# Kernel tuning notes

Hardware: AMD Instinct MI355X
Metric: run time of the kernel (lower is better)

## Reference

```python
import jax, jax.numpy as jnp
import numpy as np

HEADS = 12


def setup_inputs() -> dict:
    key = jax.random.key(0)
    ks = jax.random.split(key, 3)
    B, N, C = 4, 2048, 768
    x = jax.random.normal(ks[0], (B, N, C), dtype=jnp.float32)
    Wqkv = jax.random.normal(ks[1], (C, 3 * C), dtype=jnp.float32) * 0.02
    bqkv = jnp.zeros((3 * C,), dtype=jnp.float32)
    Wproj = jax.random.normal(ks[2], (C, C), dtype=jnp.float32) * 0.02
    bproj = jnp.zeros((C,), dtype=jnp.float32)
    return {"x": x, "Wqkv": Wqkv, "bqkv": bqkv, "Wproj": Wproj, "bproj": bproj}


def reference(x, Wqkv, bqkv, Wproj, bproj):
    B, N, C = x.shape
    h = HEADS
    d = C // h
    scale = d ** (-0.5)
    # QKV projection: (B, N, 3C) -> (3, B, h, N, d)
    qkv = (x @ Wqkv + bqkv).reshape(B, N, 3, h, d).transpose(2, 0, 3, 1, 4)
    q, k, v = qkv[0], qkv[1], qkv[2]
    # Full N x N attention scores per head (matches original explicit matmul)
    scores = jnp.einsum("bhnd,bhmd->bhnm", q, k) * scale
    attn = jax.nn.softmax(scores, axis=-1)
    out = jnp.einsum("bhnm,bhmd->bhnd", attn, v)  # (B, h, N, d)
    out = out.transpose(0, 2, 1, 3).reshape(B, N, C)
    return out @ Wproj + bproj
```

## Files before the change

### kernel.cpp

```cpp
#include <hip/hip_runtime.h>
#include <hip/hip_bf16.h>
#include <math.h>

#define B_ 4
#define N_ 2048
#define C_ 768
#define H_ 12
#define D_ 64
#define SC_LOG2E 0.18033688f

typedef __attribute__((ext_vector_type(8))) short bf16x8;
typedef __attribute__((ext_vector_type(4))) short bf16x4;
typedef __attribute__((ext_vector_type(4))) float f32x4;

#define MFMA16(A, B, C)  __builtin_amdgcn_mfma_f32_16x16x32_bf16(A, B, C, 0, 0, 0)
#define MFMAK16(A, B, C) __builtin_amdgcn_mfma_f32_16x16x16bf16_1k(A, B, C, 0, 0, 0)

#if __has_builtin(__builtin_amdgcn_exp2f)
#define EXP2F(x) __builtin_amdgcn_exp2f(x)
#else
#define EXP2F(x) exp2f(x)
#endif

__device__ __forceinline__ ushort f2bf(float f) {
    union { float f; unsigned u; } v; v.f = f;
    unsigned r = v.u + 0x7fffu + ((v.u >> 16) & 1u);
    return (ushort)(r >> 16);
}

#if __has_builtin(__builtin_amdgcn_cvt_pk_bf16_f32)
typedef __attribute__((ext_vector_type(2))) __bf16 bf16x2v;
__device__ __forceinline__ unsigned pack_bf2(float a, float b) {
    union { bf16x2v v; unsigned u; } cv;
    cv.v = __builtin_amdgcn_cvt_pk_bf16_f32(a, b);
    return cv.u;
}
#else
__device__ __forceinline__ unsigned pack_bf2(float a, float b) {
    union { __hip_bfloat162 h2; unsigned u; } cv;
    cv.h2 = __float22bfloat162_rn(make_float2(a, b));
    return cv.u;
}
#endif

__device__ __forceinline__ void gl_lds16(const ushort* g, ushort* l) {
    __builtin_amdgcn_global_load_lds(
        (const __attribute__((address_space(1))) unsigned*)g,
        (__attribute__((address_space(3))) unsigned*)l, 16, 0, 0);
}

__global__ __launch_bounds__(256) void cvt_x(const float* __restrict__ x,
                                             ushort* __restrict__ xb) {
    int i = blockIdx.x * 256 + threadIdx.x;
    const float4* p = (const float4*)x + 2 * (size_t)i;
    float4 a = p[0], bq = p[1];
    union { ushort s[8]; uint4 v; } u;
    u.s[0] = f2bf(a.x);  u.s[1] = f2bf(a.y);  u.s[2] = f2bf(a.z);  u.s[3] = f2bf(a.w);
    u.s[4] = f2bf(bq.x); u.s[5] = f2bf(bq.y); u.s[6] = f2bf(bq.z); u.s[7] = f2bf(bq.w);
    *(uint4*)&xb[(size_t)i * 8] = u.v;
}

__global__ __launch_bounds__(256) void tr_cvt(const float* __restrict__ W,
                                              ushort* __restrict__ Wt, int K, int N) {
    __shared__ float T[32][33];
    int t = threadIdx.x;
    int k0 = blockIdx.y * 32, n0 = blockIdx.x * 32;
    int r = t >> 3, c4 = (t & 7) * 4;
    float4 v = *(const float4*)&W[(size_t)(k0 + r) * N + n0 + c4];
    T[r][c4] = v.x; T[r][c4 + 1] = v.y; T[r][c4 + 2] = v.z; T[r][c4 + 3] = v.w;
    __syncthreads();
    union { ushort s[4]; unsigned long long u; } o;
    o.s[0] = f2bf(T[c4 + 0][r]);
    o.s[1] = f2bf(T[c4 + 1][r]);
    o.s[2] = f2bf(T[c4 + 2][r]);
    o.s[3] = f2bf(T[c4 + 3][r]);
    *(unsigned long long*)&Wt[(size_t)(n0 + r) * K + k0 + c4] = o.u;
}

__global__ __launch_bounds__(256) void vtrans(const ushort* __restrict__ qkvb,
                                              ushort* __restrict__ Vt) {
    __shared__ ushort T[64 * 64];
    const int tid = threadIdx.x;
    const int t0 = blockIdx.x * 64, bh = blockIdx.y;
    const int b = bh / H_, h = bh % H_;
#pragma unroll
    for (int i = 0; i < 2; i++) {
        int c = i * 256 + tid;
        int tok = c >> 3, dc = c & 7;
        uint4 v = *(const uint4*)&qkvb[((size_t)b * N_ + t0 + tok) * (3 * C_)
                                       + 2 * C_ + h * D_ + dc * 8];
        const ushort* vs = (const ushort*)&v;
#pragma unroll
        for (int j = 0; j < 8; j++) {
            int d = dc * 8 + j;
            int sc = (tok >> 3) ^ (d & 7) ^ (d >> 3);
            T[d * 64 + sc * 8 + (tok & 7)] = vs[j];
        }
    }
    __syncthreads();
#pragma unroll
    for (int i = 0; i < 2; i++) {
        int c = i * 256 + tid;
        int d = c >> 3, tc = c & 7;
        int sc = tc ^ (d & 7) ^ (d >> 3);
        uint4 o = *(const uint4*)&T[d * 64 + sc * 8];
        *(uint4*)&Vt[((size_t)bh * D_ + d) * N_ + t0 + tc * 8] = o;
    }
}

template <bool OBF>
__global__ __launch_bounds__(256) void gemm_bf16(
    const ushort* __restrict__ A, const ushort* __restrict__ Bt,
    const float* __restrict__ bias, void* __restrict__ outp,
    int M, int N, int K)
{
    __shared__ ushort Asl[128 * 32];
    __shared__ ushort Bsl[128 * 32];

    const int tid  = threadIdx.x;
    const int lane = tid & 63, w = tid >> 6;
    const int quad = lane >> 4, l16 = lane & 15;
    const int row0 = blockIdx.y * 128, col0 = blockIdx.x * 128;
    const int mh = (w >> 1) * 64, nh = (w & 1) * 64;
    const int sw = (quad ^ (l16 & 3)) * 8;

    f32x4 acc[4][4];
#pragma unroll
    for (int i = 0; i < 4; i++)
#pragma unroll
        for (int j = 0; j < 4; j++) acc[i][j] = (f32x4)0.f;

    for (int k0 = 0; k0 < K; k0 += 32) {
#pragma unroll
        for (int i = 0; i < 2; i++) {
            int c  = i * 256 + w * 64 + lane;
            int rr = c >> 2;
            int cc = (c & 3) ^ (rr & 3);
            int wb = (i * 256 + w * 64) * 8;
            gl_lds16(&A[(size_t)(row0 + rr) * K + k0 + cc * 8], &Asl[wb]);
            gl_lds16(&Bt[(size_t)(col0 + rr) * K + k0 + cc * 8], &Bsl[wb]);
        }
        __syncthreads();
        bf16x8 af[4], bfr[4];
#pragma unroll
        for (int mt = 0; mt < 4; mt++)
            af[mt] = *(const bf16x8*)&Asl[(mh + mt * 16 + l16) * 32 + sw];
#pragma unroll
        for (int nt = 0; nt < 4; nt++)
            bfr[nt] = *(const bf16x8*)&Bsl[(nh + nt * 16 + l16) * 32 + sw];
#pragma unroll
        for (int mt = 0; mt < 4; mt++)
#pragma unroll
            for (int nt = 0; nt < 4; nt++)
                acc[mt][nt] = MFMA16(af[mt], bfr[nt], acc[mt][nt]);
        __syncthreads();
    }

    const float scl = (OBF && col0 < C_) ? SC_LOG2E : 1.f;
#pragma unroll
    for (int nt = 0; nt < 4; nt++) {
        int col = col0 + nh + nt * 16 + l16;
        float bv = bias[col];
#pragma unroll
        for (int mt = 0; mt < 4; mt++) {
            f32x4 v = acc[mt][nt];
#pragma unroll
            for (int r = 0; r < 4; r++) {
                int row = row0 + mh + mt * 16 + quad * 4 + r;
                if (OBF)
                    ((ushort*)outp)[(size_t)row * N + col] = f2bf((v[r] + bv) * scl);
                else
                    ((float*)outp)[(size_t)row * N + col] = v[r] + bv;
            }
        }
    }
}

__global__ __launch_bounds__(256) void attn_mfma(
    const ushort* __restrict__ qkvb, const ushort* __restrict__ Vt,
    ushort* __restrict__ attnb)
{
    __shared__ ushort Kd[2][64 * 64];
    __shared__ ushort Vd[2][64 * 64];

    const int tid  = threadIdx.x;
    const int lane = tid & 63, w = tid >> 6;
    const int quad = lane >> 4, l16 = lane & 15;
    const int bh = blockIdx.y, b = bh / H_, h = bh % H_;
    const int q0 = blockIdx.x * 128 + w * 32;
    const size_t rowbase = (size_t)b * N_;
    const int hoff = h * D_;
    const f32x4 Z4 = {0.f, 0.f, 0.f, 0.f};

    const ushort* Kg = qkvb + rowbase * (3 * C_) + C_ + hoff;
    const ushort* Vg = Vt + (size_t)bh * D_ * N_;

    int rr0, cc0, rr1, cc1, wb0, wb1;
    {
        int c0 = w * 64 + lane, c1 = 256 + w * 64 + lane;
        rr0 = c0 >> 3; cc0 = (c0 & 7) ^ (rr0 & 7); wb0 = (w * 64) * 8;
        rr1 = c1 >> 3; cc1 = (c1 & 7) ^ (rr1 & 7); wb1 = (256 + w * 64) * 8;
    }
    const ushort* kp0 = Kg + (size_t)rr0 * (3 * C_) + cc0 * 8;
    const ushort* kp1 = Kg + (size_t)rr1 * (3 * C_) + cc1 * 8;
    const ushort* vp0 = Vg + (size_t)rr0 * N_ + cc0 * 8;
    const ushort* vp1 = Vg + (size_t)rr1 * N_ + cc1 * 8;

    bf16x8 Qf[2][2];
#pragma unroll
    for (int qt = 0; qt < 2; qt++)
#pragma unroll
        for (int c = 0; c < 2; c++)
            Qf[qt][c] = *(const bf16x8*)&qkvb[(rowbase + q0 + qt * 16 + l16) * (3 * C_)
                                              + hoff + c * 32 + quad * 8];

    f32x4 oacc[4][2];
#pragma unroll
    for (int dt = 0; dt < 4; dt++)
#pragma unroll
        for (int qt = 0; qt < 2; qt++) oacc[dt][qt] = (f32x4)0.f;
    float lrow[2] = {0.f, 0.f};

    gl_lds16(kp0, &Kd[0][wb0]);
    gl_lds16(vp0, &Vd[0][wb0]);
    gl_lds16(kp1, &Kd[0][wb1]);
    gl_lds16(vp1, &Vd[0][wb1]);
    kp0 += 64 * 3 * C_; kp1 += 64 * 3 * C_; vp0 += 64; vp1 += 64;
    __syncthreads();

#define TILE_BODY(CB, PREFETCH)                                               \
    {                                                                         \
        if (PREFETCH) {                                                       \
            gl_lds16(kp0, &Kd[(CB) ^ 1][wb0]);                                \
            gl_lds16(vp0, &Vd[(CB) ^ 1][wb0]);                                \
            gl_lds16(kp1, &Kd[(CB) ^ 1][wb1]);                                \
            gl_lds16(vp1, &Vd[(CB) ^ 1][wb1]);                                \
        }                                                                     \
        kp0 += 64 * 3 * C_; kp1 += 64 * 3 * C_; vp0 += 64; vp1 += 64;         \
        f32x4 sacc[4][2];                                                     \
        {                              \
            bf16x8 kf[4];                                                     \
            _Pragma("unroll")                                                 \
            for (int kt = 0; kt < 4; kt++)                                    \
                kf[kt] = *(const bf16x8*)&Kd[CB][(kt * 16 + l16) * 64         \
                                               + ((quad) ^ (l16 & 7)) * 8];   \
            _Pragma("unroll")                                                 \
            for (int kt = 0; kt < 4; kt++)                                    \
                _Pragma("unroll")                                             \
                for (int qt = 0; qt < 2; qt++)                                \
                    sacc[kt][qt] = MFMA16(kf[kt], Qf[qt][0], Z4);             \
        }                                                                     \
        {                                            \
            bf16x8 kf[4];                                                     \
            _Pragma("unroll")                                                 \
            for (int kt = 0; kt < 4; kt++)                                    \
                kf[kt] = *(const bf16x8*)&Kd[CB][(kt * 16 + l16) * 64         \
                                               + ((4 | quad) ^ (l16 & 7)) * 8]; \
            _Pragma("unroll")                                                 \
            for (int kt = 0; kt < 4; kt++)                                    \
                _Pragma("unroll")                                             \
                for (int qt = 0; qt < 2; qt++)                                \
                    sacc[kt][qt] = MFMA16(kf[kt], Qf[qt][1], sacc[kt][qt]);   \
        }                                                                     \
        union { unsigned u[2]; bf16x4 v; } pf[2][4];                          \
        _Pragma("unroll")                                                     \
        for (int qt = 0; qt < 2; qt++) {                                      \
            float sum = 0.f;                                                  \
            _Pragma("unroll")                                                 \
            for (int kt = 0; kt < 4; kt++) {                                  \
                float p0 = EXP2F(sacc[kt][qt][0]);                            \
                float p1 = EXP2F(sacc[kt][qt][1]);                            \
                float p2 = EXP2F(sacc[kt][qt][2]);                            \
                float p3 = EXP2F(sacc[kt][qt][3]);                            \
                sum += (p0 + p1) + (p2 + p3);                                 \
                pf[qt][kt].u[0] = pack_bf2(p0, p1);                           \
                pf[qt][kt].u[1] = pack_bf2(p2, p3);                           \
            }                                                                 \
            lrow[qt] += sum;                                                  \
        }                                                                     \
        _Pragma("unroll")                                                     \
        for (int c16 = 0; c16 < 4; c16++) {                                   \
               \
            const int vcol = ((2 * c16 + (quad >> 1)) ^ (l16 & 7)) * 8        \
                             + (quad & 1) * 4;                                \
            _Pragma("unroll")                                                 \
            for (int dt = 0; dt < 4; dt++) {                                  \
                bf16x4 vf = *(const bf16x4*)&Vd[CB][(dt * 16 + l16) * 64 + vcol]; \
                _Pragma("unroll")                                             \
                for (int qt = 0; qt < 2; qt++)                                \
                    oacc[dt][qt] = MFMAK16(vf, pf[qt][c16].v, oacc[dt][qt]);  \
            }                                                                 \
        }                                                                     \
        __syncthreads();                                                      \
    }

    for (int tt = 0; tt < 16; tt++) {
        TILE_BODY(0, 1)
        TILE_BODY(1, (tt < 15))
    }
#undef TILE_BODY

#pragma unroll
    for (int qt = 0; qt < 2; qt++) {
        float s = lrow[qt];
        s += __shfl_xor(s, 16, 64);
        s += __shfl_xor(s, 32, 64);
        float inv = 1.f / s;
        size_t orow = (rowbase + q0 + qt * 16 + l16) * C_ + hoff;
#pragma unroll
        for (int dt = 0; dt < 4; dt++) {
            union { ushort us[4]; unsigned long long u; } o;
#pragma unroll
            for (int r = 0; r < 4; r++) o.us[r] = f2bf(oacc[dt][qt][r] * inv);
            *(unsigned long long*)&attnb[orow + dt * 16 + quad * 4] = o.u;
        }
    }
}

extern "C" void kernel_launch(void* const* d_in, const int* in_sizes, int n_in,
                              void* d_out, int out_size, void* d_ws, size_t ws_size,
                              hipStream_t stream)
{
    const float* x     = (const float*)d_in[0];
    const float* Wqkv  = (const float*)d_in[1];
    const float* bqkv  = (const float*)d_in[2];
    const float* Wproj = (const float*)d_in[3];
    const float* bproj = (const float*)d_in[4];

    ushort* xb     = (ushort*)d_ws;
    ushort* Wqkvt  = xb + (size_t)B_ * N_ * C_;
    ushort* Wprojt = Wqkvt + (size_t)3 * C_ * C_;
    ushort* qkvb   = Wprojt + (size_t)C_ * C_;
    ushort* attnb  = qkvb + (size_t)B_ * N_ * 3 * C_;
    ushort* Vtb    = attnb + (size_t)B_ * N_ * C_;

    const int M = B_ * N_;

    cvt_x<<<(M * C_) / (8 * 256), 256, 0, stream>>>(x, xb);
    tr_cvt<<<dim3((3 * C_) / 32, C_ / 32), 256, 0, stream>>>(Wqkv, Wqkvt, C_, 3 * C_);
    tr_cvt<<<dim3(C_ / 32, C_ / 32), 256, 0, stream>>>(Wproj, Wprojt, C_, C_);

    gemm_bf16<true><<<dim3((3 * C_) / 128, M / 128), 256, 0, stream>>>(
        xb, Wqkvt, bqkv, qkvb, M, 3 * C_, C_);

    vtrans<<<dim3(N_ / 64, B_ * H_), 256, 0, stream>>>(qkvb, Vtb);

    attn_mfma<<<dim3(N_ / 128, B_ * H_), 256, 0, stream>>>(qkvb, Vtb, attnb);

    gemm_bf16<false><<<dim3(C_ / 128, M / 128), 256, 0, stream>>>(
        attnb, Wprojt, bproj, d_out, M, C_, C_);
}
```

Before: 252.6 us.

## Stage P through LDS for K=32 MFMA in PV and merge prep kernels

The three prep kernels (x conversion and two weight transposes) are merged into one launch that dispatches on block index, removing two launch gaps. In attention, P probabilities are written to a per-wave padded LDS tile and read back in 8-element fragments. This lets the PV product use the 16x16x32 bf16 MFMA with 8-wide V loads in place of the 16x16x16 variant with 4-wide loads, halving the MFMA count for that product. The cost is extra LDS traffic and a write-then-read round trip for P within each wave, plus extra LDS footprint.

Result: no change. 248.9 us (-1.5%).

```diff
diff --git a/kernel.cpp b/kernel.cpp
--- a/kernel.cpp
+++ b/kernel.cpp
@@ -10,11 +10,9 @@
 #define SC_LOG2E 0.18033688f
 
 typedef __attribute__((ext_vector_type(8))) short bf16x8;
-typedef __attribute__((ext_vector_type(4))) short bf16x4;
 typedef __attribute__((ext_vector_type(4))) float f32x4;
 
-#define MFMA16(A, B, C)  __builtin_amdgcn_mfma_f32_16x16x32_bf16(A, B, C, 0, 0, 0)
-#define MFMAK16(A, B, C) __builtin_amdgcn_mfma_f32_16x16x16bf16_1k(A, B, C, 0, 0, 0)
+#define MFMA16(A, B, C) __builtin_amdgcn_mfma_f32_16x16x32_bf16(A, B, C, 0, 0, 0)
 
 #if __has_builtin(__builtin_amdgcn_exp2f)
 #define EXP2F(x) __builtin_amdgcn_exp2f(x)
@@ -49,22 +47,11 @@
         (__attribute__((address_space(3))) unsigned*)l, 16, 0, 0);
 }
 
-__global__ __launch_bounds__(256) void cvt_x(const float* __restrict__ x,
-                                             ushort* __restrict__ xb) {
-    int i = blockIdx.x * 256 + threadIdx.x;
-    const float4* p = (const float4*)x + 2 * (size_t)i;
-    float4 a = p[0], bq = p[1];
-    union { ushort s[8]; uint4 v; } u;
-    u.s[0] = f2bf(a.x);  u.s[1] = f2bf(a.y);  u.s[2] = f2bf(a.z);  u.s[3] = f2bf(a.w);
-    u.s[4] = f2bf(bq.x); u.s[5] = f2bf(bq.y); u.s[6] = f2bf(bq.z); u.s[7] = f2bf(bq.w);
-    *(uint4*)&xb[(size_t)i * 8] = u.v;
-}
-
-__global__ __launch_bounds__(256) void tr_cvt(const float* __restrict__ W,
-                                              ushort* __restrict__ Wt, int K, int N) {
+__device__ __forceinline__ void tr_body(const float* __restrict__ W,
+                                        ushort* __restrict__ Wt,
+                                        int K, int N, int bx, int by, int t) {
     __shared__ float T[32][33];
-    int t = threadIdx.x;
-    int k0 = blockIdx.y * 32, n0 = blockIdx.x * 32;
+    int k0 = by * 32, n0 = bx * 32;
     int r = t >> 3, c4 = (t & 7) * 4;
     float4 v = *(const float4*)&W[(size_t)(k0 + r) * N + n0 + c4];
     T[r][c4] = v.x; T[r][c4 + 1] = v.y; T[r][c4 + 2] = v.z; T[r][c4 + 3] = v.w;
@@ -77,6 +64,29 @@
     *(unsigned long long*)&Wt[(size_t)(n0 + r) * K + k0 + c4] = o.u;
 }
 
+__global__ __launch_bounds__(256) void prep(
+    const float* __restrict__ x, ushort* __restrict__ xb,
+    const float* __restrict__ Wqkv, ushort* __restrict__ Wqkvt,
+    const float* __restrict__ Wproj, ushort* __restrict__ Wprojt)
+{
+    const int bid = blockIdx.x, t = threadIdx.x;
+    if (bid < 3072) {
+        int i = bid * 256 + t;
+        const float4* p = (const float4*)x + 2 * (size_t)i;
+        float4 a = p[0], bq = p[1];
+        union { ushort s[8]; uint4 v; } u;
+        u.s[0] = f2bf(a.x);  u.s[1] = f2bf(a.y);  u.s[2] = f2bf(a.z);  u.s[3] = f2bf(a.w);
+        u.s[4] = f2bf(bq.x); u.s[5] = f2bf(bq.y); u.s[6] = f2bf(bq.z); u.s[7] = f2bf(bq.w);
+        *(uint4*)&xb[(size_t)i * 8] = u.v;
+    } else if (bid < 4800) {
+        int id = bid - 3072;
+        tr_body(Wqkv, Wqkvt, C_, 3 * C_, id % 72, id / 72, t);
+    } else {
+        int id = bid - 4800;
+        tr_body(Wproj, Wprojt, C_, C_, id % 24, id / 24, t);
+    }
+}
+
 __global__ __launch_bounds__(256) void vtrans(const ushort* __restrict__ qkvb,
                                               ushort* __restrict__ Vt) {
     __shared__ ushort T[64 * 64];
@@ -182,6 +192,7 @@
 {
     __shared__ ushort Kd[2][64 * 64];
     __shared__ ushort Vd[2][64 * 64];
+    __shared__ ushort Ptl[4 * 32 * 72];
 
     const int tid  = threadIdx.x;
     const int lane = tid & 63, w = tid >> 6;
@@ -190,6 +201,7 @@
     const int q0 = blockIdx.x * 128 + w * 32;
     const size_t rowbase = (size_t)b * N_;
     const int hoff = h * D_;
+    ushort* Ptw = Ptl + w * 32 * 72;
     const f32x4 Z4 = {0.f, 0.f, 0.f, 0.f};
 
     const ushort* Kg = qkvb + rowbase * (3 * C_) + C_ + hoff;
@@ -238,7 +250,7 @@
         }                                                                     \
         kp0 += 64 * 3 * C_; kp1 += 64 * 3 * C_; vp0 += 64; vp1 += 64;         \
         f32x4 sacc[4][2];                                                     \
-        {                              \
+        {                                \
             bf16x8 kf[4];                                                     \
             _Pragma("unroll")                                                 \
             for (int kt = 0; kt < 4; kt++)                                    \
@@ -250,7 +262,7 @@
                 for (int qt = 0; qt < 2; qt++)                                \
                     sacc[kt][qt] = MFMA16(kf[kt], Qf[qt][0], Z4);             \
         }                                                                     \
-        {                                            \
+        {                                              \
             bf16x8 kf[4];                                                     \
             _Pragma("unroll")                                                 \
             for (int kt = 0; kt < 4; kt++)                                    \
@@ -262,7 +274,6 @@
                 for (int qt = 0; qt < 2; qt++)                                \
                     sacc[kt][qt] = MFMA16(kf[kt], Qf[qt][1], sacc[kt][qt]);   \
         }                                                                     \
-        union { unsigned u[2]; bf16x4 v; } pf[2][4];                          \
         _Pragma("unroll")                                                     \
         for (int qt = 0; qt < 2; qt++) {                                      \
             float sum = 0.f;                                                  \
@@ -273,22 +284,27 @@
                 float p2 = EXP2F(sacc[kt][qt][2]);                            \
                 float p3 = EXP2F(sacc[kt][qt][3]);                            \
                 sum += (p0 + p1) + (p2 + p3);                                 \
-                pf[qt][kt].u[0] = pack_bf2(p0, p1);                           \
-                pf[qt][kt].u[1] = pack_bf2(p2, p3);                           \
+                uint2 pk;                                                     \
+                pk.x = pack_bf2(p0, p1);                                      \
+                pk.y = pack_bf2(p2, p3);                                      \
+                *(uint2*)&Ptw[(qt * 16 + l16) * 72 + kt * 16 + quad * 4] = pk; \
             }                                                                 \
             lrow[qt] += sum;                                                  \
         }                                                                     \
         _Pragma("unroll")                                                     \
-        for (int c16 = 0; c16 < 4; c16++) {                                   \
-               \
-            const int vcol = ((2 * c16 + (quad >> 1)) ^ (l16 & 7)) * 8        \
-                             + (quad & 1) * 4;                                \
+        for (int c = 0; c < 2; c++) {                                         \
+            bf16x8 pf[2];                                                     \
+            _Pragma("unroll")                                                 \
+            for (int qt = 0; qt < 2; qt++)                                    \
+                pf[qt] = *(const bf16x8*)&Ptw[(qt * 16 + l16) * 72            \
+                                              + c * 32 + quad * 8];           \
             _Pragma("unroll")                                                 \
             for (int dt = 0; dt < 4; dt++) {                                  \
-                bf16x4 vf = *(const bf16x4*)&Vd[CB][(dt * 16 + l16) * 64 + vcol]; \
+                bf16x8 vf = *(const bf16x8*)&Vd[CB][(dt * 16 + l16) * 64      \
+                                   + (((c << 2) | quad) ^ (l16 & 7)) * 8];    \
                 _Pragma("unroll")                                             \
                 for (int qt = 0; qt < 2; qt++)                                \
-                    oacc[dt][qt] = MFMAK16(vf, pf[qt][c16].v, oacc[dt][qt]);  \
+                    oacc[dt][qt] = MFMA16(vf, pf[qt], oacc[dt][qt]);          \
             }                                                                 \
         }                                                                     \
         __syncthreads();                                                      \
@@ -336,9 +352,7 @@
 
     const int M = B_ * N_;
 
-    cvt_x<<<(M * C_) / (8 * 256), 256, 0, stream>>>(x, xb);
-    tr_cvt<<<dim3((3 * C_) / 32, C_ / 32), 256, 0, stream>>>(Wqkv, Wqkvt, C_, 3 * C_);
-    tr_cvt<<<dim3(C_ / 32, C_ / 32), 256, 0, stream>>>(Wproj, Wprojt, C_, C_);
+    prep<<<5376, 256, 0, stream>>>(x, xb, Wqkv, Wqkvt, Wproj, Wprojt);
 
     gemm_bf16<true><<<dim3((3 * C_) / 128, M / 128), 256, 0, stream>>>(
         xb, Wqkvt, bqkv, qkvb, M, 3 * C_, C_);
```
